# Optimization experiments

Measured on AMD Instinct MI355X. Metric: run time of the kernel, lower is better.

The kernel has to match this reference:

```python
import jax, jax.numpy as jnp
import numpy as np

B, S, D, H = 2, 2048, 1024, 16
HD = D // H

def setup_inputs() -> dict:
    key = jax.random.key(0)
    ks = jax.random.split(key, 9)
    s = 1.0 / np.sqrt(D)
    inp = {"x": jax.random.normal(ks[0], (B, S, D), dtype=jnp.float32)}
    for i, name in enumerate(["q", "k", "v", "o"]):
        inp[f"W_{name}"] = jax.random.uniform(ks[1 + 2 * i], (D, D), dtype=jnp.float32, minval=-s, maxval=s)
        inp[f"b_{name}"] = jax.random.uniform(ks[2 + 2 * i], (D,), dtype=jnp.float32, minval=-s, maxval=s)
    return inp


def reference(x, W_q, b_q, W_k, b_k, W_v, b_v, W_o, b_o):
    # x: [B, S, D]
    def split_heads(t):
        return t.reshape(B, S, H, HD).transpose(0, 2, 1, 3)  # [B, H, S, HD]

    Q = split_heads(x @ W_q + b_q)
    K = split_heads(x @ W_k + b_k)
    V = split_heads(x @ W_v + b_v)

    scale = 1.0 / np.sqrt(HD).astype(np.float32)
    scores = jnp.einsum("bhqd,bhkd->bhqk", Q, K) * scale  # [B, H, S, S]
    weights = jax.nn.softmax(scores, axis=-1)
    attn = jnp.einsum("bhqk,bhkd->bhqd", weights, V)  # [B, H, S, HD]
    attn = attn.transpose(0, 2, 1, 3).reshape(B, S, D)
    return attn @ W_o + b_o
```

## Files before the change

### kernel.cpp

```cpp
#include <hip/hip_runtime.h>
#include <hip/hip_bf16.h>

#define BB 2
#define SS 2048
#define DD 1024
#define HH 16
#define HD 64

typedef __attribute__((ext_vector_type(8))) short bf16x8;
typedef __attribute__((ext_vector_type(4))) float f32x4;

__device__ __forceinline__ unsigned short f2bf(float f) {
  unsigned int u = __float_as_uint(f);
  return (unsigned short)((u + 0x7FFFu + ((u >> 16) & 1u)) >> 16);
}

__device__ __forceinline__ float fast_exp2(float x) {
#if __has_builtin(__builtin_amdgcn_exp2f)
  return __builtin_amdgcn_exp2f(x);
#else
  return __expf(x * 0.6931471805599453f);
#endif
}

__device__ __forceinline__ void async_copy16(const unsigned short* gp, unsigned short* lp) {
  __builtin_amdgcn_global_load_lds(
      (const __attribute__((address_space(1))) unsigned int*)gp,
      (__attribute__((address_space(3))) unsigned int*)lp, 16, 0, 0);
}

__device__ __forceinline__ void pl32_swap(unsigned& a, unsigned& b) {
#if __has_builtin(__builtin_amdgcn_permlane32_swap)
  auto r = __builtin_amdgcn_permlane32_swap(a, b, false, false);
  a = r[0];
  b = r[1];
#else
  asm volatile("v_permlane32_swap_b32 %0, %1" : "+v"(a), "+v"(b));
#endif
}
__device__ __forceinline__ void pl16_swap(unsigned& a, unsigned& b) {
#if __has_builtin(__builtin_amdgcn_permlane16_swap)
  auto r = __builtin_amdgcn_permlane16_swap(a, b, false, false);
  a = r[0];
  b = r[1];
#else
  asm volatile("v_permlane16_swap_b32 %0, %1" : "+v"(a), "+v"(b));
#endif
}

__global__ __launch_bounds__(256) void prep_kernel(
    const float* __restrict__ x, unsigned short* __restrict__ xb,
    const float* __restrict__ W0, unsigned short* __restrict__ T0,
    const float* __restrict__ W1, unsigned short* __restrict__ T1,
    const float* __restrict__ W2, unsigned short* __restrict__ T2,
    const float* __restrict__ W3, unsigned short* __restrict__ T3) {
  const int blk = blockIdx.x;
  const int t = threadIdx.x;
  if (blk < 4096) {
    int i = blk * 1024 + t * 4;
    float4 v = *(const float4*)(x + i);
    ushort4 u;
    u.x = f2bf(v.x); u.y = f2bf(v.y); u.z = f2bf(v.z); u.w = f2bf(v.w);
    *(ushort4*)(xb + i) = u;
    return;
  }
  const int j = blk - 4096;
  const int jw = j >> 10;
  const int tb = j & 1023;
  const float* W = jw == 0 ? W0 : (jw == 1 ? W1 : (jw == 2 ? W2 : W3));
  unsigned short* T = jw == 0 ? T0 : (jw == 1 ? T1 : (jw == 2 ? T2 : T3));
  __shared__ float tile[32][33];
  int k0 = (tb & 31) * 32, n0 = (tb >> 5) * 32;
  int c = t & 31, r0 = t >> 5;
#pragma unroll
  for (int i = 0; i < 4; ++i) {
    int r = r0 + i * 8;
    tile[r][c] = W[(size_t)(k0 + r) * DD + n0 + c];
  }
  __syncthreads();
#pragma unroll
  for (int i = 0; i < 4; ++i) {
    int r = r0 + i * 8;
    T[(size_t)(n0 + r) * DD + k0 + c] = f2bf(tile[c][r]);
  }
}

template <int STORE>
__device__ __forceinline__ void gemm_core(
    const unsigned short* __restrict__ A, const unsigned short* __restrict__ BT,
    const float* __restrict__ bias, void* __restrict__ outp, float scale,
    int bm, int bn) {
  const int t = threadIdx.x;
  const int w = t >> 6;
  const int l = t & 63;
  const int wm = (w >> 1) * 64;
  const int wn = (w & 1) * 64;

  __shared__ __align__(16) unsigned short As[128 * 32];
  __shared__ __align__(16) unsigned short Bs[128 * 32];

  f32x4 acc[4][4];
#pragma unroll
  for (int i = 0; i < 4; ++i)
#pragma unroll
    for (int j = 0; j < 4; ++j) acc[i][j] = (f32x4)0.f;

  const int fr = l & 15;
  const int kg = (l >> 4) * 8;

  for (int k0 = 0; k0 < DD; k0 += 32) {
    __syncthreads();
#pragma unroll
    for (int c = 0; c < 2; ++c) {
      int e = (w * 2 + c) * 512 + l * 8;
      int row = e >> 5, kk = e & 31;
      async_copy16(A + (size_t)(bm + row) * DD + k0 + kk, As + (w * 2 + c) * 512);
      async_copy16(BT + (size_t)(bn + row) * DD + k0 + kk, Bs + (w * 2 + c) * 512);
    }
    __syncthreads();

    bf16x8 af[4], bfr[4];
#pragma unroll
    for (int i = 0; i < 4; ++i)
      af[i] = *(const bf16x8*)(As + (wm + i * 16 + fr) * 32 + kg);
#pragma unroll
    for (int j = 0; j < 4; ++j)
      bfr[j] = *(const bf16x8*)(Bs + (wn + j * 16 + fr) * 32 + kg);
#pragma unroll
    for (int i = 0; i < 4; ++i)
#pragma unroll
      for (int j = 0; j < 4; ++j)
        acc[i][j] = __builtin_amdgcn_mfma_f32_16x16x32_bf16(af[i], bfr[j], acc[i][j], 0, 0, 0);
  }

  const int col_l = l & 15;
  const int row_l = (l >> 4) * 4;

  if (STORE == 2) {
    unsigned short* out = (unsigned short*)outp;
    unsigned int* T = (unsigned int*)As;
    const int b_ = bm >> 11;
    const int srow0 = bm & 2047;
#pragma unroll
    for (int p = 0; p < 4; ++p) {
      __syncthreads();
      if ((w & 1) == (p >> 1)) {
        const int jt0 = (p & 1) * 2;
#pragma unroll
        for (int jj = 0; jj < 2; ++jj) {
          int jt = jt0 + jj;
          int n_p = jj * 16 + col_l;
          float bv = bias[bn + p * 32 + n_p];
#pragma unroll
          for (int i = 0; i < 4; ++i) {
            int m0 = wm + i * 16 + row_l;
#pragma unroll
            for (int pr = 0; pr < 2; ++pr) {
              unsigned int val =
                  (unsigned int)f2bf(acc[i][jt][2 * pr] + bv) |
                  ((unsigned int)f2bf(acc[i][jt][2 * pr + 1] + bv) << 16);
              int m = m0 + 2 * pr;
              T[n_p * 64 + (((m >> 1)) ^ ((n_p & 7) << 2))] = val;
            }
          }
        }
      }
      __syncthreads();
#pragma unroll
      for (int c = 0; c < 2; ++c) {
        int q = t + c * 256;
        int n_p = q >> 4, cpos = q & 15;
        uint4 v = *(const uint4*)(T + n_p * 64 + ((cpos * 4) ^ ((n_p & 7) << 2)));
        int n_glob = bn + p * 32 + n_p;
        int h_ = n_glob >> 6, hd_ = n_glob & 63;
        *(uint4*)(out + ((size_t)((b_ * HH + h_) * HD + hd_)) * SS + srow0 + cpos * 8) = v;
      }
    }
    return;
  }

#pragma unroll
  for (int i = 0; i < 4; ++i) {
    int m_base = bm + wm + i * 16 + row_l;
#pragma unroll
    for (int j = 0; j < 4; ++j) {
      int n = bn + wn + j * 16 + col_l;
      float bv = bias[n];
      if (STORE == 0) {
        float* out = (float*)outp;
#pragma unroll
        for (int r = 0; r < 4; ++r)
          out[(size_t)(m_base + r) * DD + n] = acc[i][j][r] + bv;
      } else {
        unsigned short* out = (unsigned short*)outp;
        int h_ = n >> 6, hd_ = n & 63;
#pragma unroll
        for (int r = 0; r < 4; ++r) {
          int m = m_base + r;
          int b_ = m >> 11, s_ = m & 2047;
          out[(((size_t)(b_ * HH + h_) * SS) + s_) * HD + hd_] =
              f2bf((acc[i][j][r] + bv) * scale);
        }
      }
    }
  }
}

__global__ __launch_bounds__(256) void qkv_gemm_mfma(
    const unsigned short* __restrict__ A,
    const unsigned short* __restrict__ WqT, const unsigned short* __restrict__ WkT,
    const unsigned short* __restrict__ WvT,
    const float* __restrict__ bq, const float* __restrict__ bk,
    const float* __restrict__ bv,
    unsigned short* __restrict__ Qo, unsigned short* __restrict__ Ko,
    unsigned short* __restrict__ VTo) {
  const int i = blockIdx.x;
  const int xcd = i & 7;
  const int slot = i >> 3;
  const int bm = (xcd + 8 * (slot / 24)) * 128;
  const int c = slot % 24;
  const int which = c >> 3;
  const int bn = (c & 7) * 128;
  if (which == 0)
    gemm_core<1>(A, WqT, bq, (void*)Qo, 0.18033688011112042f, bm, bn);
  else if (which == 1)
    gemm_core<1>(A, WkT, bk, (void*)Ko, 1.0f, bm, bn);
  else
    gemm_core<2>(A, WvT, bv, (void*)VTo, 1.0f, bm, bn);
}

__global__ __launch_bounds__(256) void out_gemm_mfma(
    const unsigned short* __restrict__ A, const unsigned short* __restrict__ WoT,
    const float* __restrict__ bo, float* __restrict__ out) {
  const int i = blockIdx.x;
  const int xcd = i & 7;
  const int slot = i >> 3;
  const int bm = (xcd + 8 * (slot >> 3)) * 128;
  const int bn = (slot & 7) * 128;
  gemm_core<0>(A, WoT, bo, (void*)out, 1.0f, bm, bn);
}

__global__ __launch_bounds__(256) void flash_attn_mfma(
    const unsigned short* __restrict__ Q,
    const unsigned short* __restrict__ K,
    const unsigned short* __restrict__ VT,
    unsigned short* __restrict__ ctx) {
  const int bh = blockIdx.x;
  const int qt = blockIdx.y;
  const int b  = bh >> 4;
  const int h  = bh & 15;
  const int t  = threadIdx.x;
  const int w  = t >> 6;
  const int l  = t & 63;
  const int g  = l >> 4;
  const int ln = l & 15;

  const unsigned short* Qp = Q + ((size_t)bh * SS + (size_t)qt * 128 + w * 32) * HD;
  const unsigned short* Kp = K + (size_t)bh * SS * HD;
  const unsigned short* Vp = VT + (size_t)bh * HD * SS;

  __shared__ __align__(16) unsigned short Ks[2][64 * 64];
  __shared__ __align__(16) unsigned short Vs[2][64 * 64];

  bf16x8 qf[2][2];
#pragma unroll
  for (int nt = 0; nt < 2; ++nt)
#pragma unroll
    for (int kb = 0; kb < 2; ++kb)
      qf[nt][kb] = *(const bf16x8*)(Qp + (nt * 16 + ln) * HD + kb * 32 + g * 8);

  f32x4 o[2][4];
#pragma unroll
  for (int nt = 0; nt < 2; ++nt)
#pragma unroll
    for (int mt = 0; mt < 4; ++mt) o[nt][mt] = (f32x4)0.f;
  float rs[2] = {0.f, 0.f};

  auto stage = [&](int kt, int half) {
#pragma unroll
    for (int j = 0; j < 2; ++j) {
      int c = (w * 2 + j) * 64 + l;
      int row = c >> 3, cc = c & 7;
      int gcc = cc ^ (row & 7);
      async_copy16(Kp + (size_t)(kt * 64 + row) * HD + gcc * 8,
                   &Ks[half][(w * 2 + j) * 512]);
      async_copy16(Vp + (size_t)row * SS + kt * 64 + gcc * 8,
                   &Vs[half][(w * 2 + j) * 512]);
    }
  };

  stage(0, 0);
  for (int kt = 0; kt < SS / 64; ++kt) {
    const int half = kt & 1;
    __syncthreads();
    if (kt + 1 < SS / 64) stage(kt + 1, half ^ 1);

    f32x4 st[2][4];
#pragma unroll
    for (int nt = 0; nt < 2; ++nt)
#pragma unroll
      for (int mt = 0; mt < 4; ++mt) st[nt][mt] = (f32x4)0.f;
#pragma unroll
    for (int kb = 0; kb < 2; ++kb)
#pragma unroll
      for (int mt = 0; mt < 4; ++mt) {
        int row = mt * 16 + ln;
        bf16x8 ka = *(const bf16x8*)(&Ks[half][row * 64 + (((kb * 4 + g) ^ (row & 7)) * 8)]);
        st[0][mt] = __builtin_amdgcn_mfma_f32_16x16x32_bf16(ka, qf[0][kb], st[0][mt], 0, 0, 0);
        st[1][mt] = __builtin_amdgcn_mfma_f32_16x16x32_bf16(ka, qf[1][kb], st[1][mt], 0, 0, 0);
      }

    unsigned Sd[2][4][2];
#pragma unroll
    for (int nt = 0; nt < 2; ++nt) {
#pragma unroll
      for (int mt = 0; mt < 4; ++mt) {
        float p0 = fast_exp2(st[nt][mt][0]);
        float p1 = fast_exp2(st[nt][mt][1]);
        float p2 = fast_exp2(st[nt][mt][2]);
        float p3 = fast_exp2(st[nt][mt][3]);
        Sd[nt][mt][0] = __builtin_amdgcn_perm(__float_as_uint(p1), __float_as_uint(p0),
                                              0x07060302u);
        Sd[nt][mt][1] = __builtin_amdgcn_perm(__float_as_uint(p3), __float_as_uint(p2),
                                              0x07060302u);
        rs[nt] += (p0 + p1) + (p2 + p3);
      }
#pragma unroll
      for (int m1 = 0; m1 < 2; ++m1)
#pragma unroll
        for (int p = 0; p < 2; ++p)
          pl32_swap(Sd[nt][2 * m1][p], Sd[nt][2 * m1 + 1][p]);
#pragma unroll
      for (int m1 = 0; m1 < 2; ++m1)
#pragma unroll
        for (int p = 0; p < 2; ++p)
          pl16_swap(Sd[nt][2 * m1][p], Sd[nt][2 * m1 + 1][p]);
    }

#pragma unroll
    for (int kb = 0; kb < 2; ++kb) {
      bf16x8 pbv[2];
#pragma unroll
      for (int nt = 0; nt < 2; ++nt) {
        union { unsigned u[4]; bf16x8 v; } c;
        c.u[0] = Sd[nt][2 * kb][0];
        c.u[1] = Sd[nt][2 * kb][1];
        c.u[2] = Sd[nt][2 * kb + 1][0];
        c.u[3] = Sd[nt][2 * kb + 1][1];
        pbv[nt] = c.v;
      }
#pragma unroll
      for (int mt = 0; mt < 4; ++mt) {
        int row = mt * 16 + ln;
        bf16x8 va = *(const bf16x8*)(&Vs[half][row * 64 + (((kb * 4 + g) ^ (row & 7)) * 8)]);
        o[0][mt] = __builtin_amdgcn_mfma_f32_16x16x32_bf16(va, pbv[0], o[0][mt], 0, 0, 0);
        o[1][mt] = __builtin_amdgcn_mfma_f32_16x16x32_bf16(va, pbv[1], o[1][mt], 0, 0, 0);
      }
    }
  }

#pragma unroll
  for (int nt = 0; nt < 2; ++nt) {
    float lsum = rs[nt];
    lsum += __shfl_xor(lsum, 16, 64);
    lsum += __shfl_xor(lsum, 32, 64);
    float inv = 1.f / lsum;
    int srow = qt * 128 + w * 32 + nt * 16 + ln;
    unsigned short* cb = ctx + (size_t)(b * SS + srow) * DD + h * HD;
#pragma unroll
    for (int mt = 0; mt < 4; ++mt) {
      ushort4 u4;
      u4.x = f2bf(o[nt][mt][0] * inv);
      u4.y = f2bf(o[nt][mt][1] * inv);
      u4.z = f2bf(o[nt][mt][2] * inv);
      u4.w = f2bf(o[nt][mt][3] * inv);
      *(ushort4*)(cb + mt * 16 + 4 * g) = u4;
    }
  }
}

extern "C" void kernel_launch(void* const* d_in, const int* in_sizes, int n_in,
                              void* d_out, int out_size, void* d_ws, size_t ws_size,
                              hipStream_t stream) {
  const float* x  = (const float*)d_in[0];
  const float* Wq = (const float*)d_in[1];
  const float* bq = (const float*)d_in[2];
  const float* Wk = (const float*)d_in[3];
  const float* bk = (const float*)d_in[4];
  const float* Wv = (const float*)d_in[5];
  const float* bv = (const float*)d_in[6];
  const float* Wo = (const float*)d_in[7];
  const float* bo = (const float*)d_in[8];
  float* out = (float*)d_out;

  const size_t ELEMS = (size_t)BB * SS * DD;
  char* ws = (char*)d_ws;
  unsigned short* xb   = (unsigned short*)ws;  ws += ELEMS * 2;
  unsigned short* WqT  = (unsigned short*)ws;  ws += (size_t)DD * DD * 2;
  unsigned short* WkT  = (unsigned short*)ws;  ws += (size_t)DD * DD * 2;
  unsigned short* WvT  = (unsigned short*)ws;  ws += (size_t)DD * DD * 2;
  unsigned short* WoT  = (unsigned short*)ws;  ws += (size_t)DD * DD * 2;
  unsigned short* Qb   = (unsigned short*)ws;  ws += ELEMS * 2;
  unsigned short* Kb   = (unsigned short*)ws;  ws += ELEMS * 2;
  unsigned short* VbT  = (unsigned short*)ws;  ws += ELEMS * 2;
  unsigned short* ctxb = (unsigned short*)ws;  ws += ELEMS * 2;

  prep_kernel<<<8192, 256, 0, stream>>>(x, xb, Wq, WqT, Wk, WkT, Wv, WvT, Wo, WoT);

  qkv_gemm_mfma<<<768, 256, 0, stream>>>(xb, WqT, WkT, WvT, bq, bk, bv,
                                         Qb, Kb, VbT);

  dim3 attn_grid(BB * HH, SS / 128);
  flash_attn_mfma<<<attn_grid, 256, 0, stream>>>(Qb, Kb, VbT, ctxb);

  out_gemm_mfma<<<256, 256, 0, stream>>>(ctxb, WoT, bo, out);
}
```

Before: 210.2 us.

## Split attention key range across two wave groups with shared-memory reduction

Doubles the flash-attention block to 512 threads. Two groups of four waves each process alternating 64-key halves of a 128-key staged tile for the same 128 queries. Partial outputs and row sums are then combined through shared memory before the final normalisation. The aim is more waves in flight per query tile to hide latency, at the cost of double the LDS footprint, an extra reduction pass and higher register pressure under the launch-bounds hint.

```diff
diff --git a/kernel.cpp b/kernel.cpp
--- a/kernel.cpp
+++ b/kernel.cpp
@@ -240,7 +240,7 @@
   gemm_core<0>(A, WoT, bo, (void*)out, 1.0f, bm, bn);
 }
 
-__global__ __launch_bounds__(256) void flash_attn_mfma(
+__global__ __launch_bounds__(512, 4) void flash_attn_mfma(
     const unsigned short* __restrict__ Q,
     const unsigned short* __restrict__ K,
     const unsigned short* __restrict__ VT,
@@ -252,15 +252,17 @@
   const int t  = threadIdx.x;
   const int w  = t >> 6;
   const int l  = t & 63;
+  const int wg = w & 3;
+  const int wh = w >> 2;
   const int g  = l >> 4;
   const int ln = l & 15;
 
-  const unsigned short* Qp = Q + ((size_t)bh * SS + (size_t)qt * 128 + w * 32) * HD;
+  const unsigned short* Qp = Q + ((size_t)bh * SS + (size_t)qt * 128 + wg * 32) * HD;
   const unsigned short* Kp = K + (size_t)bh * SS * HD;
   const unsigned short* Vp = VT + (size_t)bh * HD * SS;
 
-  __shared__ __align__(16) unsigned short Ks[2][64 * 64];
-  __shared__ __align__(16) unsigned short Vs[2][64 * 64];
+  __shared__ __align__(16) unsigned short Ks[2][2][64 * 64];
+  __shared__ __align__(16) unsigned short Vs[2][2][64 * 64];
 
   bf16x8 qf[2][2];
 #pragma unroll
@@ -276,24 +278,29 @@
     for (int mt = 0; mt < 4; ++mt) o[nt][mt] = (f32x4)0.f;
   float rs[2] = {0.f, 0.f};
 
-  auto stage = [&](int kt, int half) {
-#pragma unroll
-    for (int j = 0; j < 2; ++j) {
-      int c = (w * 2 + j) * 64 + l;
-      int row = c >> 3, cc = c & 7;
-      int gcc = cc ^ (row & 7);
-      async_copy16(Kp + (size_t)(kt * 64 + row) * HD + gcc * 8,
-                   &Ks[half][(w * 2 + j) * 512]);
-      async_copy16(Vp + (size_t)row * SS + kt * 64 + gcc * 8,
-                   &Vs[half][(w * 2 + j) * 512]);
-    }
+  auto stage2 = [&](int kt2, int db) {
+    const int c = t;
+    const int row = c >> 3, cc = c & 7;
+    const int gcc = cc ^ (row & 7);
+    const int k0 = kt2 * 128;
+    unsigned short* dK0 = &Ks[0][db][w * 512];
+    unsigned short* dK1 = &Ks[1][db][w * 512];
+    unsigned short* dV0 = &Vs[0][db][w * 512];
+    unsigned short* dV1 = &Vs[1][db][w * 512];
+    async_copy16(Kp + (size_t)(k0 + row) * HD + gcc * 8, dK0);
+    async_copy16(Kp + (size_t)(k0 + 64 + row) * HD + gcc * 8, dK1);
+    async_copy16(Vp + (size_t)row * SS + k0 + gcc * 8, dV0);
+    async_copy16(Vp + (size_t)row * SS + k0 + 64 + gcc * 8, dV1);
   };
 
-  stage(0, 0);
-  for (int kt = 0; kt < SS / 64; ++kt) {
-    const int half = kt & 1;
+  stage2(0, 0);
+  for (int kt2 = 0; kt2 < SS / 128; ++kt2) {
+    const int db = kt2 & 1;
     __syncthreads();
-    if (kt + 1 < SS / 64) stage(kt + 1, half ^ 1);
+    if (kt2 + 1 < SS / 128) stage2(kt2 + 1, db ^ 1);
+
+    const unsigned short* Kst = &Ks[wh][db][0];
+    const unsigned short* Vst = &Vs[wh][db][0];
 
     f32x4 st[2][4];
 #pragma unroll
@@ -305,7 +312,7 @@
 #pragma unroll
       for (int mt = 0; mt < 4; ++mt) {
         int row = mt * 16 + ln;
-        bf16x8 ka = *(const bf16x8*)(&Ks[half][row * 64 + (((kb * 4 + g) ^ (row & 7)) * 8)]);
+        bf16x8 ka = *(const bf16x8*)(&Kst[row * 64 + (((kb * 4 + g) ^ (row & 7)) * 8)]);
         st[0][mt] = __builtin_amdgcn_mfma_f32_16x16x32_bf16(ka, qf[0][kb], st[0][mt], 0, 0, 0);
         st[1][mt] = __builtin_amdgcn_mfma_f32_16x16x32_bf16(ka, qf[1][kb], st[1][mt], 0, 0, 0);
       }
@@ -352,11 +359,42 @@
 #pragma unroll
       for (int mt = 0; mt < 4; ++mt) {
         int row = mt * 16 + ln;
-        bf16x8 va = *(const bf16x8*)(&Vs[half][row * 64 + (((kb * 4 + g) ^ (row & 7)) * 8)]);
+        bf16x8 va = *(const bf16x8*)(&Vst[row * 64 + (((kb * 4 + g) ^ (row & 7)) * 8)]);
         o[0][mt] = __builtin_amdgcn_mfma_f32_16x16x32_bf16(va, pbv[0], o[0][mt], 0, 0, 0);
         o[1][mt] = __builtin_amdgcn_mfma_f32_16x16x32_bf16(va, pbv[1], o[1][mt], 0, 0, 0);
       }
     }
+  }
+
+  __syncthreads();
+  {
+    float* ored = (float*)&Vs[0][0][0];
+    float* rred = (float*)&Ks[0][0][0];
+    float* rb = ored + (wg * 64 + l) * 32;
+    float* sb = rred + (wg * 64 + l) * 2;
+    if (wh == 1) {
+#pragma unroll
+      for (int nt = 0; nt < 2; ++nt)
+#pragma unroll
+        for (int mt = 0; mt < 4; ++mt) {
+          int idx = nt * 4 + mt;
+          *(f32x4*)(rb + ((unsigned)(idx ^ (l & 7)) * 4)) = o[nt][mt];
+        }
+      sb[0] = rs[0];
+      sb[1] = rs[1];
+    }
+    __syncthreads();
+    if (wh == 1) return;
+#pragma unroll
+    for (int nt = 0; nt < 2; ++nt)
+#pragma unroll
+      for (int mt = 0; mt < 4; ++mt) {
+        int idx = nt * 4 + mt;
+        f32x4 pv = *(const f32x4*)(rb + ((unsigned)(idx ^ (l & 7)) * 4));
+        o[nt][mt] += pv;
+      }
+    rs[0] += sb[0];
+    rs[1] += sb[1];
   }
 
 #pragma unroll
@@ -365,7 +403,7 @@
     lsum += __shfl_xor(lsum, 16, 64);
     lsum += __shfl_xor(lsum, 32, 64);
     float inv = 1.f / lsum;
-    int srow = qt * 128 + w * 32 + nt * 16 + ln;
+    int srow = qt * 128 + wg * 32 + nt * 16 + ln;
     unsigned short* cb = ctx + (size_t)(b * SS + srow) * DD + h * HD;
 #pragma unroll
     for (int mt = 0; mt < 4; ++mt) {
@@ -411,7 +449,7 @@
                                          Qb, Kb, VbT);
 
   dim3 attn_grid(BB * HH, SS / 128);
-  flash_attn_mfma<<<attn_grid, 256, 0, stream>>>(Qb, Kb, VbT, ctxb);
+  flash_attn_mfma<<<attn_grid, 512, 0, stream>>>(Qb, Kb, VbT, ctxb);
 
   out_gemm_mfma<<<256, 256, 0, stream>>>(ctxb, WoT, bo, out);
 }
```

Measured after the change: 201.1 us. 1.04x faster.
